# Kernel tuning notes

Measured on AMD Instinct MI355X. Metric: run time of the kernel, lower is better.

Reference implementation:

```python
import jax, jax.numpy as jnp
import numpy as np

DIMS = 256; K = 3; G = 4; CG = DIMS // G; P = K * K
STRIDE = 1; PAD = K // 2; DIL = 1; OFFSET_SCALE = 1.0; SOFTMAX = False
PW_OUT = int(np.ceil(G * P * 3 / 8) * 8)  # 112


def setup_inputs() -> dict:
    key = jax.random.key(0)
    ks = jax.random.split(key, 6)
    N, H, W = 4, 64, 64
    x = jax.random.normal(ks[0], (N, DIMS, H, W), dtype=jnp.float32)
    dw_w = jax.random.normal(ks[1], (DIMS, 1, K, K), dtype=jnp.float32) * 0.1
    dw_b = jnp.zeros((DIMS,), dtype=jnp.float32)
    pw_w = jax.random.normal(ks[2], (PW_OUT, DIMS), dtype=jnp.float32) * 0.01
    pw_b = jnp.zeros((PW_OUT,), dtype=jnp.float32)
    pin_w = jax.random.normal(ks[3], (DIMS, DIMS), dtype=jnp.float32) * (1.0 / np.sqrt(DIMS))
    pin_b = jnp.zeros((DIMS,), dtype=jnp.float32)
    pout_w = jax.random.normal(ks[4], (DIMS, DIMS), dtype=jnp.float32) * (1.0 / np.sqrt(DIMS))
    pout_b = jnp.zeros((DIMS,), dtype=jnp.float32)
    return {"x": x, "dw_w": dw_w, "dw_b": dw_b, "pw_w": pw_w, "pw_b": pw_b,
            "pin_w": pin_w, "pin_b": pin_b, "pout_w": pout_w, "pout_b": pout_b}


def _forward(x, dw_w, dw_b, pw_w, pw_b, pin_w, pin_b, pout_w, pout_b):
    N, C, H, W = x.shape
    L = H * W
    inp = x.reshape(N, C, L).transpose(0, 2, 1)              # [N, L, C]
    # input projection
    val = inp @ pin_w.T + pin_b                               # [N, L, C]
    # offset/mask head: depthwise conv (on raw input) + pointwise linear
    om = jax.lax.conv_general_dilated(
        x, dw_w, window_strides=(1, 1), padding=[(PAD, PAD), (PAD, PAD)],
        dimension_numbers=("NCHW", "OIHW", "NCHW"), feature_group_count=C)
    om = om + dw_b[None, :, None, None]
    om = om.reshape(N, C, L).transpose(0, 2, 1)               # [N, L, C]
    om = om @ pw_w.T + pw_b                                   # [N, L, PW_OUT]
    om = om[..., : G * P * 3].reshape(N, L, G, P, 3)
    off_x = om[..., 0] * OFFSET_SCALE                         # [N, L, G, P]
    off_y = om[..., 1] * OFFSET_SCALE
    mask = om[..., 2]
    if SOFTMAX:
        mask = jax.nn.softmax(mask, axis=-1)
    # kernel grid (P points)
    ky, kx = jnp.meshgrid(jnp.arange(K), jnp.arange(K), indexing="ij")
    ky = (ky.reshape(-1) * DIL).astype(jnp.float32)           # [P]
    kx = (kx.reshape(-1) * DIL).astype(jnp.float32)
    # base output positions (stride 1, zero pad)
    yb = jnp.repeat(jnp.arange(H), W).astype(jnp.float32) * STRIDE - PAD   # [L]
    xb = jnp.tile(jnp.arange(W), H).astype(jnp.float32) * STRIDE - PAD
    pos_y = yb[None, :, None, None] + ky[None, None, None, :] + off_y     # [N,L,G,P]
    pos_x = xb[None, :, None, None] + kx[None, None, None, :] + off_x
    # bilinear gather from grouped value tensor
    vflat = val.reshape(N * L * G, CG)
    n_ids = jnp.arange(N)[:, None, None, None]
    g_ids = jnp.arange(G)[None, None, :, None]

    def gather(iy, ix):
        valid = (iy >= 0) & (iy < H) & (ix >= 0) & (ix < W)
        sidx = jnp.clip(iy, 0, H - 1) * W + jnp.clip(ix, 0, W - 1)
        gidx = (n_ids * L + sidx) * G + g_ids                 # [N,L,G,P]
        v = vflat[gidx]                                       # [N,L,G,P,CG]
        return jnp.where(valid[..., None], v, 0.0)

    y0 = jnp.floor(pos_y); x0 = jnp.floor(pos_x)
    fy = pos_y - y0; fx = pos_x - x0
    iy0 = y0.astype(jnp.int32); ix0 = x0.astype(jnp.int32)
    iy1 = iy0 + 1; ix1 = ix0 + 1
    w00 = (1 - fy) * (1 - fx); w01 = (1 - fy) * fx
    w10 = fy * (1 - fx); w11 = fy * fx
    acc = (jnp.einsum("nlgp,nlgpc->nlgc", mask * w00, gather(iy0, ix0))
           + jnp.einsum("nlgp,nlgpc->nlgc", mask * w01, gather(iy0, ix1))
           + jnp.einsum("nlgp,nlgpc->nlgc", mask * w10, gather(iy1, ix0))
           + jnp.einsum("nlgp,nlgpc->nlgc", mask * w11, gather(iy1, ix1)))
    out = acc.reshape(N, L, C)
    out = out @ pout_w.T + pout_b                             # output projection
    return out.transpose(0, 2, 1).reshape(N, C, H, W)


def reference(x, dw_w, dw_b, pw_w, pw_b, pin_w, pin_b, pout_w, pout_b):
    return _forward(x, dw_w, dw_b, pw_w, pw_b, pin_w, pin_b, pout_w, pout_b)
```

## Files before the change

kernel.cpp:

```cpp
#include <hip/hip_runtime.h>

typedef unsigned short u16;
typedef short bf16x8 __attribute__((ext_vector_type(8)));
typedef u16 u16x8 __attribute__((ext_vector_type(8)));
typedef float f32x4 __attribute__((ext_vector_type(4)));

#define K_DIM 256
#define L_DIM 4096
#define NBATCH 4

static __device__ __forceinline__ u16 f2bf(float f) {
    unsigned u = __float_as_uint(f);
    unsigned r = (u + 0x7FFFu + ((u >> 16) & 1u)) >> 16;
    return (u16)r;
}
static __device__ __forceinline__ float bf2f(u16 v) {
    return __uint_as_float(((unsigned)v) << 16);
}

#define GLOAD16(g, l) __builtin_amdgcn_global_load_lds( \
    (const __attribute__((address_space(1))) void*)(g), \
    (__attribute__((address_space(3))) void*)(l), 16, 0, 0)

__global__ __launch_bounds__(256) void prep_kernel(
    const float* __restrict__ x, const float* __restrict__ dw_w,
    const float* __restrict__ dw_b, const float* __restrict__ pin_w,
    const float* __restrict__ pw_w, const float* __restrict__ pout_w,
    u16* __restrict__ xb_t, u16* __restrict__ dwc_t,
    u16* __restrict__ pin_wb, u16* __restrict__ pw_wb,
    u16* __restrict__ pout_wb)
{
    if (blockIdx.x == 4) {
        if (blockIdx.z != 0) return;
        const int end = (blockIdx.y + 1) * 2560;
        for (int k = blockIdx.y * 2560 + threadIdx.x; k < end; k += 256) {
            if (k < 65536) pin_wb[k] = f2bf(pin_w[k]);
            else if (k < 98304) {
                int j = k - 65536;
                pw_wb[j] = ((j >> 8) < 112) ? f2bf(pw_w[j]) : (u16)0;
            } else {
                int j = k - 98304;
                pout_wb[j] = f2bf(pout_w[j]);
            }
        }
        return;
    }

    __shared__ u16 tx_[64][66];
    __shared__ u16 td_[64][66];
    const int c0 = blockIdx.x * 64, h = blockIdx.y, n = blockIdx.z;
    const int t = threadIdx.x;
    const float* xn = x + (size_t)n * 256 * L_DIM;

    const int w4 = (t & 15) * 4;
    const int cs = t >> 4;

    #pragma unroll
    for (int j = 0; j < 4; ++j) {
        const int cl = cs * 4 + j, c = c0 + cl;
        const float* xc = xn + (size_t)c * L_DIM;
        const float* w9 = dw_w + c * 9;

        float s[4];
        const float bv = dw_b[c];
        #pragma unroll
        for (int k = 0; k < 4; ++k) s[k] = bv;
        f32x4 center;

        #pragma unroll
        for (int dy = 0; dy < 3; ++dy) {
            const int hh = h + dy - 1;
            if (hh < 0 || hh > 63) continue;
            const float* row = xc + hh * 64;
            const f32x4 m = *(const f32x4*)(row + w4);
            const float flv = row[(w4 > 0) ? w4 - 1 : 0];
            const float frv = row[(w4 + 4 < 64) ? w4 + 4 : 63];
            if (dy == 1) center = m;
            #pragma unroll
            for (int k = 0; k < 4; ++k) {
                const int w = w4 + k;
                const float lv = (w > 0) ? 1.f : 0.f;
                const float rv = (w < 63) ? 1.f : 0.f;
                const float xm = (k == 0) ? flv : m[k - 1];
                const float xp = (k == 3) ? frv : m[k + 1];
                s[k] = fmaf(xm * lv, w9[dy*3 + 0], s[k]);
                s[k] = fmaf(m[k],    w9[dy*3 + 1], s[k]);
                s[k] = fmaf(xp * rv, w9[dy*3 + 2], s[k]);
            }
        }
        #pragma unroll
        for (int k = 0; k < 4; ++k) {
            tx_[w4 + k][cl] = f2bf(center[k]);
            td_[w4 + k][cl] = f2bf(s[k]);
        }
    }
    __syncthreads();

    const int cc = t & 63, cq = t >> 6;
    for (int j = 0; j < 16; ++j) {
        const int wl = j * 4 + cq;
        const size_t o = ((size_t)n * L_DIM + h * 64 + wl) * 256 + c0 + cc;
        xb_t[o]  = tx_[wl][cc];
        dwc_t[o] = td_[wl][cc];
    }
}

__global__ __launch_bounds__(256) void gemm_dual(
    const u16* __restrict__ xb_t, const u16* __restrict__ dwc_t,
    const u16* __restrict__ pin_wb, const u16* __restrict__ pw_wb,
    const float* __restrict__ pin_b, const float* __restrict__ pw_b,
    u16* __restrict__ val_b, float* __restrict__ omb)
{
    __shared__ u16 lds[16384];
    const int bx = blockIdx.x;
    const bool isPw = (bx == 2);
    const u16* Ag = isPw ? dwc_t : xb_t;
    const u16* Bg = isPw ? pw_wb : pin_wb;
    const float* bias = isPw ? pw_b : pin_b;
    const int n0 = isPw ? 0 : bx * 128;
    const int Ncols = isPw ? 112 : 256;
    const int ldC = isPw ? 112 : 256;
    const int m0 = blockIdx.y * 128;

    const int t = threadIdx.x;
    const int wave = t >> 6, lane = t & 63;
    const int lr = lane & 15, lk = lane >> 4;
    const int wr = wave >> 1, wc = wave & 1;
    const int wbase = wave << 10;

    const int srow = t >> 2;
    const int scol = (t & 3) * 8;
    const u16* ga0 = Ag + (size_t)(m0 + srow)      * K_DIM + scol;
    const u16* ga1 = Ag + (size_t)(m0 + 64 + srow) * K_DIM + scol;
    const u16* gb0 = Bg + (size_t)(n0 + srow)      * K_DIM + scol;
    const u16* gb1 = Bg + (size_t)(n0 + 64 + srow) * K_DIM + scol;

    f32x4 acc[4][4];
    #pragma unroll
    for (int m = 0; m < 4; ++m)
        #pragma unroll
        for (int n = 0; n < 4; ++n) acc[m][n] = (f32x4){0.f, 0.f, 0.f, 0.f};

    auto stage = [&](int b, int kt) {
        const int ko = kt * 32;
        char* base = (char*)lds + b * 16384 + wbase;
        GLOAD16(ga0 + ko, base);
        GLOAD16(ga1 + ko, base + 4096);
        GLOAD16(gb0 + ko, base + 8192);
        GLOAD16(gb1 + ko, base + 12288);
    };

    stage(0, 0);
    asm volatile("s_waitcnt vmcnt(0)" ::: "memory");
    __syncthreads();

    for (int kt = 0; kt < 8; ++kt) {
        const int cur = kt & 1;
        if (kt < 7) stage(cur ^ 1, kt + 1);
        const char* la = (const char*)lds + cur * 16384;
        const char* lb = la + 8192;
        bf16x8 af[4], bfr[4];
        #pragma unroll
        for (int m = 0; m < 4; ++m)
            af[m] = *(const bf16x8*)(la + ((wr*64 + m*16 + lr) * 32 + lk * 8) * 2);
        #pragma unroll
        for (int n = 0; n < 4; ++n)
            bfr[n] = *(const bf16x8*)(lb + ((wc*64 + n*16 + lr) * 32 + lk * 8) * 2);
        #pragma unroll
        for (int m = 0; m < 4; ++m)
            #pragma unroll
            for (int n = 0; n < 4; ++n)
                acc[m][n] = __builtin_amdgcn_mfma_f32_16x16x32_bf16(
                    af[m], bfr[n], acc[m][n], 0, 0, 0);
        asm volatile("s_waitcnt vmcnt(0)" ::: "memory");
        __syncthreads();
    }

    #pragma unroll
    for (int m = 0; m < 4; ++m) {
        #pragma unroll
        for (int n = 0; n < 4; ++n) {
            const int col = n0 + wc*64 + n*16 + lr;
            if (col < Ncols) {
                const float bv = bias[col];
                #pragma unroll
                for (int r = 0; r < 4; ++r) {
                    const int row = m0 + wr*64 + m*16 + lk*4 + r;
                    const float o = acc[m][n][r] + bv;
                    const size_t off = (size_t)row * ldC + col;
                    if (isPw) omb[off] = o;
                    else      val_b[off] = f2bf(o);
                }
            }
        }
    }
}

__global__ __launch_bounds__(512, 4) void gather_pout(
    const float* __restrict__ om, const u16* __restrict__ val,
    const u16* __restrict__ pout_wb, const float* __restrict__ pout_b,
    float* __restrict__ out)
{
    __shared__ u16 sacc[32][264];
    __shared__ float som[4096];
    const int blk = blockIdx.x;
    const int xcd = blk & 7, s = blk >> 3;
    const int half = s & 1, rd = (s >> 1) & 7, n = s >> 4;
    const int h = xcd * 8 + rd;
    const int l0 = h * 64 + half * 32;
    const int t = threadIdx.x;

    {
        const float* omsrc = om + ((size_t)n * L_DIM + l0) * 112;
        const int wb = (t >> 6) << 10;
        GLOAD16(omsrc + t * 4,        (char*)som + wb);
        GLOAD16(omsrc + 2048 + t * 4, (char*)som + 8192 + wb);
        asm volatile("s_waitcnt vmcnt(0)" ::: "memory");
        __syncthreads();
    }

    {
        const u16* valn = val + (size_t)n * L_DIM * 256;
        const float ybase = (float)h - 1.f;

        #pragma unroll
        for (int i = 0; i < 2; ++i) {
            const int slot = i * 512 + t;
            const int pos = slot >> 5;
            const int g = (slot >> 3) & 3;
            const int ch = (slot & 7) * 8;
            const int l = l0 + pos;
            const float* omp = som + pos * 112 + g * 27;
            const u16* vb = valn + g * 64 + ch;
            const float xb = (float)(l & 63) - 1.f;

            float a[8];
            #pragma unroll
            for (int j = 0; j < 8; ++j) a[j] = 0.f;

            #pragma unroll 3
            for (int p = 0; p < 9; ++p) {
                const float ox = omp[p*3 + 0];
                const float oy = omp[p*3 + 1];
                const float mk = omp[p*3 + 2];
                const float py = ybase + (float)(p / 3) + oy;
                const float px = xb + (float)(p % 3) + ox;
                const float y0 = floorf(py), x0 = floorf(px);
                const float fy = py - y0, fx = px - x0;
                const int iy0 = (int)y0, ix0 = (int)x0;
                const float wy[2] = {mk * (1.f - fy), mk * fy};
                const float wx[2] = {1.f - fx, fx};
                #pragma unroll
                for (int c4 = 0; c4 < 4; ++c4) {
                    const int dy = c4 >> 1, dx = c4 & 1;
                    const int iy = iy0 + dy, ix = ix0 + dx;
                    const bool ok = ((unsigned)iy < 64u) & ((unsigned)ix < 64u);
                    const float wgt = ok ? wy[dy] * wx[dx] : 0.f;
                    const int iyc = min(max(iy, 0), 63);
                    const int ixc = min(max(ix, 0), 63);
                    const u16x8 v = *(const u16x8*)(vb + (size_t)(iyc * 64 + ixc) * 256);
                    #pragma unroll
                    for (int j = 0; j < 8; ++j) a[j] = fmaf(wgt, bf2f(v[j]), a[j]);
                }
            }
            u16x8 o;
            #pragma unroll
            for (int j = 0; j < 8; ++j) o[j] = f2bf(a[j]);
            *(u16x8*)(&sacc[pos][g*64 + ch]) = o;
        }
    }
    __syncthreads();

    const int wave = t >> 6, lane = t & 63;
    const int lr = lane & 15, lk = lane >> 4;

    f32x4 acc4[2][2];
    #pragma unroll
    for (int m = 0; m < 2; ++m)
        #pragma unroll
        for (int nn = 0; nn < 2; ++nn) acc4[m][nn] = (f32x4){0.f, 0.f, 0.f, 0.f};

    #pragma unroll
    for (int kt = 0; kt < 8; ++kt) {
        bf16x8 bfr[2];
        #pragma unroll
        for (int nn = 0; nn < 2; ++nn)
            bfr[nn] = *(const bf16x8*)(&sacc[nn*16 + lr][kt*32 + lk*8]);
        #pragma unroll
        for (int m = 0; m < 2; ++m) {
            const bf16x8 af = *(const bf16x8*)(pout_wb +
                (size_t)(wave*32 + m*16 + lr) * K_DIM + kt*32 + lk*8);
            #pragma unroll
            for (int nn = 0; nn < 2; ++nn)
                acc4[m][nn] = __builtin_amdgcn_mfma_f32_16x16x32_bf16(
                    af, bfr[nn], acc4[m][nn], 0, 0, 0);
        }
    }

    float* outn = out + (size_t)n * 256 * L_DIM;
    #pragma unroll
    for (int m = 0; m < 2; ++m) {
        #pragma unroll
        for (int nn = 0; nn < 2; ++nn) {
            const int col = l0 + nn*16 + lr;
            #pragma unroll
            for (int r = 0; r < 4; ++r) {
                const int row = wave*32 + m*16 + lk*4 + r;
                outn[(size_t)row * L_DIM + col] = acc4[m][nn][r] + pout_b[row];
            }
        }
    }
}

extern "C" void kernel_launch(void* const* d_in, const int* in_sizes, int n_in,
                              void* d_out, int out_size, void* d_ws, size_t ws_size,
                              hipStream_t stream) {
    const float* x      = (const float*)d_in[0];
    const float* dw_w   = (const float*)d_in[1];
    const float* dw_b   = (const float*)d_in[2];
    const float* pw_w   = (const float*)d_in[3];
    const float* pw_b   = (const float*)d_in[4];
    const float* pin_w  = (const float*)d_in[5];
    const float* pin_b  = (const float*)d_in[6];
    const float* pout_w = (const float*)d_in[7];
    const float* pout_b = (const float*)d_in[8];
    float* out = (float*)d_out;

    char* ws = (char*)d_ws;
    u16*   xb_t    = (u16*)ws;
    u16*   dwc_t   = (u16*)(ws + 8388608);
    u16*   val_b   = (u16*)(ws + 16777216);
    float* omb     = (float*)(ws + 25165824);
    u16*   pin_wb  = (u16*)(ws + 32505856);
    u16*   pw_wb   = (u16*)(ws + 32636928);
    u16*   pout_wb = (u16*)(ws + 32702464);

    prep_kernel<<<dim3(5, 64, NBATCH), 256, 0, stream>>>(
        x, dw_w, dw_b, pin_w, pw_w, pout_w,
        xb_t, dwc_t, pin_wb, pw_wb, pout_wb);

    gemm_dual<<<dim3(3, 128), 256, 0, stream>>>(
        xb_t, dwc_t, pin_wb, pw_wb, pin_b, pw_b, val_b, omb);

    gather_pout<<<dim3(512), 512, 0, stream>>>(
        omb, val_b, pout_wb, pout_b, out);
}
```

Before: 58.13 us.

## Fuse offset/mask pointwise GEMM into gather kernel, drop om round-trip

Moves the 112-column pointwise projection of the depthwise conv output out of the dual GEMM kernel and computes it inside gather_pout with MFMA, writing straight to LDS. The input GEMM now launches only the pin-projection blocks. This removes the fp32 om buffer write and reread through global memory and shrinks the GEMM grid, in exchange for extra work and global loads at the start of each gather block, which happen before the gather itself can begin.

```diff
diff --git a/kernel.cpp b/kernel.cpp
--- a/kernel.cpp
+++ b/kernel.cpp
@@ -105,21 +105,12 @@
     }
 }
 
-__global__ __launch_bounds__(256) void gemm_dual(
-    const u16* __restrict__ xb_t, const u16* __restrict__ dwc_t,
-    const u16* __restrict__ pin_wb, const u16* __restrict__ pw_wb,
-    const float* __restrict__ pin_b, const float* __restrict__ pw_b,
-    u16* __restrict__ val_b, float* __restrict__ omb)
+__global__ __launch_bounds__(256) void gemm_pin(
+    const u16* __restrict__ xb_t, const u16* __restrict__ pin_wb,
+    const float* __restrict__ pin_b, u16* __restrict__ val_b)
 {
     __shared__ u16 lds[16384];
-    const int bx = blockIdx.x;
-    const bool isPw = (bx == 2);
-    const u16* Ag = isPw ? dwc_t : xb_t;
-    const u16* Bg = isPw ? pw_wb : pin_wb;
-    const float* bias = isPw ? pw_b : pin_b;
-    const int n0 = isPw ? 0 : bx * 128;
-    const int Ncols = isPw ? 112 : 256;
-    const int ldC = isPw ? 112 : 256;
+    const int n0 = blockIdx.x * 128;
     const int m0 = blockIdx.y * 128;
 
     const int t = threadIdx.x;
@@ -130,10 +121,10 @@
 
     const int srow = t >> 2;
     const int scol = (t & 3) * 8;
-    const u16* ga0 = Ag + (size_t)(m0 + srow)      * K_DIM + scol;
-    const u16* ga1 = Ag + (size_t)(m0 + 64 + srow) * K_DIM + scol;
-    const u16* gb0 = Bg + (size_t)(n0 + srow)      * K_DIM + scol;
-    const u16* gb1 = Bg + (size_t)(n0 + 64 + srow) * K_DIM + scol;
+    const u16* ga0 = xb_t + (size_t)(m0 + srow)      * K_DIM + scol;
+    const u16* ga1 = xb_t + (size_t)(m0 + 64 + srow) * K_DIM + scol;
+    const u16* gb0 = pin_wb + (size_t)(n0 + srow)      * K_DIM + scol;
+    const u16* gb1 = pin_wb + (size_t)(n0 + 64 + srow) * K_DIM + scol;
 
     f32x4 acc[4][4];
     #pragma unroll
@@ -181,43 +172,58 @@
         #pragma unroll
         for (int n = 0; n < 4; ++n) {
             const int col = n0 + wc*64 + n*16 + lr;
-            if (col < Ncols) {
-                const float bv = bias[col];
-                #pragma unroll
-                for (int r = 0; r < 4; ++r) {
-                    const int row = m0 + wr*64 + m*16 + lk*4 + r;
-                    const float o = acc[m][n][r] + bv;
-                    const size_t off = (size_t)row * ldC + col;
-                    if (isPw) omb[off] = o;
-                    else      val_b[off] = f2bf(o);
-                }
+            const float bv = pin_b[col];
+            #pragma unroll
+            for (int r = 0; r < 4; ++r) {
+                const int row = m0 + wr*64 + m*16 + lk*4 + r;
+                val_b[(size_t)row * 256 + col] = f2bf(acc[m][n][r] + bv);
             }
         }
     }
 }
 
 __global__ __launch_bounds__(512, 4) void gather_pout(
-    const float* __restrict__ om, const u16* __restrict__ val,
+    const u16* __restrict__ dwc_t, const u16* __restrict__ val,
+    const u16* __restrict__ pw_wb, const float* __restrict__ pw_b,
     const u16* __restrict__ pout_wb, const float* __restrict__ pout_b,
     float* __restrict__ out)
 {
     __shared__ u16 sacc[32][264];
-    __shared__ float som[4096];
+    __shared__ float som[32 * 112];
     const int blk = blockIdx.x;
     const int xcd = blk & 7, s = blk >> 3;
     const int half = s & 1, rd = (s >> 1) & 7, n = s >> 4;
     const int h = xcd * 8 + rd;
     const int l0 = h * 64 + half * 32;
     const int t = threadIdx.x;
+    const int wave = t >> 6, lane = t & 63;
+    const int lr = lane & 15, lk = lane >> 4;
 
     {
-        const float* omsrc = om + ((size_t)n * L_DIM + l0) * 112;
-        const int wb = (t >> 6) << 10;
-        GLOAD16(omsrc + t * 4,        (char*)som + wb);
-        GLOAD16(omsrc + 2048 + t * 4, (char*)som + 8192 + wb);
-        asm volatile("s_waitcnt vmcnt(0)" ::: "memory");
-        __syncthreads();
-    }
+        const u16* dwcn = dwc_t + ((size_t)n * L_DIM + l0) * 256;
+        #pragma unroll
+        for (int tt = 0; tt < 2; ++tt) {
+            const int T = wave + tt * 8;
+            if (T < 14) {
+                const int m = T & 1, nn = T >> 1;
+                f32x4 acc = (f32x4){0.f, 0.f, 0.f, 0.f};
+                #pragma unroll
+                for (int kt = 0; kt < 8; ++kt) {
+                    const bf16x8 a = *(const bf16x8*)(dwcn +
+                        (size_t)(m*16 + lr) * K_DIM + kt*32 + lk*8);
+                    const bf16x8 b = *(const bf16x8*)(pw_wb +
+                        (size_t)(nn*16 + lr) * K_DIM + kt*32 + lk*8);
+                    acc = __builtin_amdgcn_mfma_f32_16x16x32_bf16(a, b, acc, 0, 0, 0);
+                }
+                const int col = nn*16 + lr;
+                const float bv = pw_b[col];
+                #pragma unroll
+                for (int r = 0; r < 4; ++r)
+                    som[(m*16 + lk*4 + r) * 112 + col] = acc[r] + bv;
+            }
+        }
+    }
+    __syncthreads();
 
     {
         const u16* valn = val + (size_t)n * L_DIM * 256;
@@ -271,9 +277,6 @@
     }
     __syncthreads();
 
-    const int wave = t >> 6, lane = t & 63;
-    const int lr = lane & 15, lk = lane >> 4;
-
     f32x4 acc4[2][2];
     #pragma unroll
     for (int m = 0; m < 2; ++m)
@@ -330,18 +333,17 @@
     u16*   xb_t    = (u16*)ws;
     u16*   dwc_t   = (u16*)(ws + 8388608);
     u16*   val_b   = (u16*)(ws + 16777216);
-    float* omb     = (float*)(ws + 25165824);
-    u16*   pin_wb  = (u16*)(ws + 32505856);
-    u16*   pw_wb   = (u16*)(ws + 32636928);
-    u16*   pout_wb = (u16*)(ws + 32702464);
+    u16*   pin_wb  = (u16*)(ws + 25165824);
+    u16*   pw_wb   = (u16*)(ws + 25296896);
+    u16*   pout_wb = (u16*)(ws + 25362432);
 
     prep_kernel<<<dim3(5, 64, NBATCH), 256, 0, stream>>>(
         x, dw_w, dw_b, pin_w, pw_w, pout_w,
         xb_t, dwc_t, pin_wb, pw_wb, pout_wb);
 
-    gemm_dual<<<dim3(3, 128), 256, 0, stream>>>(
-        xb_t, dwc_t, pin_wb, pw_wb, pin_b, pw_b, val_b, omb);
+    gemm_pin<<<dim3(2, 128), 256, 0, stream>>>(
+        xb_t, pin_wb, pin_b, val_b);
 
     gather_pout<<<dim3(512), 512, 0, stream>>>(
-        omb, val_b, pout_wb, pout_b, out);
-}
+        dwc_t, val_b, pw_wb, pw_b, pout_wb, pout_b, out);
+}
```

New measurement: 65.97 us. +13.5%, slower.

## Split fused gather+output projection into separate gather and tiled GEMM kernels

Applied to the files above, without the earlier changes.

Replaces the fused gather_pout kernel with two kernels. A small-block gather kernel writes bf16 sampled features to a workspace buffer. A separate double-buffered 128x128 MFMA GEMM then applies the output projection. This is meant to raise gather occupancy and to get better weight reuse and LDS staging in the projection GEMM. The cost is an extra global round-trip of an 8 MB intermediate and one more kernel launch.

```diff
diff --git a/kernel.cpp b/kernel.cpp
--- a/kernel.cpp
+++ b/kernel.cpp
@@ -196,117 +196,145 @@
     }
 }
 
-__global__ __launch_bounds__(512, 4) void gather_pout(
+__global__ __launch_bounds__(256, 8) void gather_kernel(
     const float* __restrict__ om, const u16* __restrict__ val,
-    const u16* __restrict__ pout_wb, const float* __restrict__ pout_b,
-    float* __restrict__ out)
+    u16* __restrict__ accb)
 {
-    __shared__ u16 sacc[32][264];
-    __shared__ float som[4096];
+    __shared__ float som[904];
     const int blk = blockIdx.x;
-    const int xcd = blk & 7, s = blk >> 3;
-    const int half = s & 1, rd = (s >> 1) & 7, n = s >> 4;
-    const int h = xcd * 8 + rd;
-    const int l0 = h * 64 + half * 32;
+    const int grp = (blk & 7) * 256 + (blk >> 3);
+    const int n = grp >> 9;
+    const int l0 = (grp & 511) * 8;
     const int t = threadIdx.x;
 
     {
         const float* omsrc = om + ((size_t)n * L_DIM + l0) * 112;
-        const int wb = (t >> 6) << 10;
-        GLOAD16(omsrc + t * 4,        (char*)som + wb);
-        GLOAD16(omsrc + 2048 + t * 4, (char*)som + 8192 + wb);
+        if (t < 224) {
+            const int wb = (t >> 6) << 10;
+            GLOAD16(omsrc + t * 4, (char*)som + wb);
+        }
         asm volatile("s_waitcnt vmcnt(0)" ::: "memory");
         __syncthreads();
     }
 
-    {
-        const u16* valn = val + (size_t)n * L_DIM * 256;
-        const float ybase = (float)h - 1.f;
-
-        #pragma unroll
-        for (int i = 0; i < 2; ++i) {
-            const int slot = i * 512 + t;
-            const int pos = slot >> 5;
-            const int g = (slot >> 3) & 3;
-            const int ch = (slot & 7) * 8;
-            const int l = l0 + pos;
-            const float* omp = som + pos * 112 + g * 27;
-            const u16* vb = valn + g * 64 + ch;
-            const float xb = (float)(l & 63) - 1.f;
-
-            float a[8];
-            #pragma unroll
-            for (int j = 0; j < 8; ++j) a[j] = 0.f;
-
-            #pragma unroll 3
-            for (int p = 0; p < 9; ++p) {
-                const float ox = omp[p*3 + 0];
-                const float oy = omp[p*3 + 1];
-                const float mk = omp[p*3 + 2];
-                const float py = ybase + (float)(p / 3) + oy;
-                const float px = xb + (float)(p % 3) + ox;
-                const float y0 = floorf(py), x0 = floorf(px);
-                const float fy = py - y0, fx = px - x0;
-                const int iy0 = (int)y0, ix0 = (int)x0;
-                const float wy[2] = {mk * (1.f - fy), mk * fy};
-                const float wx[2] = {1.f - fx, fx};
-                #pragma unroll
-                for (int c4 = 0; c4 < 4; ++c4) {
-                    const int dy = c4 >> 1, dx = c4 & 1;
-                    const int iy = iy0 + dy, ix = ix0 + dx;
-                    const bool ok = ((unsigned)iy < 64u) & ((unsigned)ix < 64u);
-                    const float wgt = ok ? wy[dy] * wx[dx] : 0.f;
-                    const int iyc = min(max(iy, 0), 63);
-                    const int ixc = min(max(ix, 0), 63);
-                    const u16x8 v = *(const u16x8*)(vb + (size_t)(iyc * 64 + ixc) * 256);
-                    #pragma unroll
-                    for (int j = 0; j < 8; ++j) a[j] = fmaf(wgt, bf2f(v[j]), a[j]);
-                }
-            }
-            u16x8 o;
-            #pragma unroll
-            for (int j = 0; j < 8; ++j) o[j] = f2bf(a[j]);
-            *(u16x8*)(&sacc[pos][g*64 + ch]) = o;
-        }
-    }
-    __syncthreads();
-
+    const int pos = t >> 5;
+    const int g = (t >> 3) & 3;
+    const int ch = (t & 7) * 8;
+    const int l = l0 + pos;
+    const float* omp = som + pos * 112 + g * 27;
+    const u16* vb = val + (size_t)n * L_DIM * 256 + g * 64 + ch;
+    const float ybase = (float)(l >> 6) - 1.f;
+    const float xb = (float)(l & 63) - 1.f;
+
+    float a[8];
+    #pragma unroll
+    for (int j = 0; j < 8; ++j) a[j] = 0.f;
+
+    #pragma unroll 3
+    for (int p = 0; p < 9; ++p) {
+        const float ox = omp[p*3 + 0];
+        const float oy = omp[p*3 + 1];
+        const float mk = omp[p*3 + 2];
+        const float py = ybase + (float)(p / 3) + oy;
+        const float px = xb + (float)(p % 3) + ox;
+        const float y0 = floorf(py), x0 = floorf(px);
+        const float fy = py - y0, fx = px - x0;
+        const int iy0 = (int)y0, ix0 = (int)x0;
+        const float wy[2] = {mk * (1.f - fy), mk * fy};
+        const float wx[2] = {1.f - fx, fx};
+        #pragma unroll
+        for (int c4 = 0; c4 < 4; ++c4) {
+            const int dy = c4 >> 1, dx = c4 & 1;
+            const int iy = iy0 + dy, ix = ix0 + dx;
+            const bool ok = ((unsigned)iy < 64u) & ((unsigned)ix < 64u);
+            const float wgt = ok ? wy[dy] * wx[dx] : 0.f;
+            const int iyc = min(max(iy, 0), 63);
+            const int ixc = min(max(ix, 0), 63);
+            const u16x8 v = *(const u16x8*)(vb + (size_t)(iyc * 64 + ixc) * 256);
+            #pragma unroll
+            for (int j = 0; j < 8; ++j) a[j] = fmaf(wgt, bf2f(v[j]), a[j]);
+        }
+    }
+    u16x8 o;
+    #pragma unroll
+    for (int j = 0; j < 8; ++j) o[j] = f2bf(a[j]);
+    *(u16x8*)(accb + ((size_t)n * L_DIM + l) * 256 + g * 64 + ch) = o;
+}
+
+__global__ __launch_bounds__(256) void gemm_pout(
+    const u16* __restrict__ accb, const u16* __restrict__ pout_wb,
+    const float* __restrict__ pout_b, float* __restrict__ out)
+{
+    __shared__ u16 lds[16384];
+    const int z = blockIdx.z;
+    const u16* Bg = accb + (size_t)z * L_DIM * 256;
+    const int n0 = blockIdx.x * 128;
+    const int m0 = blockIdx.y * 128;
+
+    const int t = threadIdx.x;
     const int wave = t >> 6, lane = t & 63;
     const int lr = lane & 15, lk = lane >> 4;
-
-    f32x4 acc4[2][2];
-    #pragma unroll
-    for (int m = 0; m < 2; ++m)
-        #pragma unroll
-        for (int nn = 0; nn < 2; ++nn) acc4[m][nn] = (f32x4){0.f, 0.f, 0.f, 0.f};
-
-    #pragma unroll
+    const int wr = wave >> 1, wc = wave & 1;
+    const int wbase = wave << 10;
+
+    const int srow = t >> 2;
+    const int scol = (t & 3) * 8;
+    const u16* ga0 = pout_wb + (size_t)(m0 + srow)      * K_DIM + scol;
+    const u16* ga1 = pout_wb + (size_t)(m0 + 64 + srow) * K_DIM + scol;
+    const u16* gb0 = Bg + (size_t)(n0 + srow)      * K_DIM + scol;
+    const u16* gb1 = Bg + (size_t)(n0 + 64 + srow) * K_DIM + scol;
+
+    f32x4 acc[4][4];
+    #pragma unroll
+    for (int m = 0; m < 4; ++m)
+        #pragma unroll
+        for (int n = 0; n < 4; ++n) acc[m][n] = (f32x4){0.f, 0.f, 0.f, 0.f};
+
+    auto stage = [&](int b, int kt) {
+        const int ko = kt * 32;
+        char* base = (char*)lds + b * 16384 + wbase;
+        GLOAD16(ga0 + ko, base);
+        GLOAD16(ga1 + ko, base + 4096);
+        GLOAD16(gb0 + ko, base + 8192);
+        GLOAD16(gb1 + ko, base + 12288);
+    };
+
+    stage(0, 0);
+    asm volatile("s_waitcnt vmcnt(0)" ::: "memory");
+    __syncthreads();
+
     for (int kt = 0; kt < 8; ++kt) {
-        bf16x8 bfr[2];
-        #pragma unroll
-        for (int nn = 0; nn < 2; ++nn)
-            bfr[nn] = *(const bf16x8*)(&sacc[nn*16 + lr][kt*32 + lk*8]);
-        #pragma unroll
-        for (int m = 0; m < 2; ++m) {
-            const bf16x8 af = *(const bf16x8*)(pout_wb +
-                (size_t)(wave*32 + m*16 + lr) * K_DIM + kt*32 + lk*8);
-            #pragma unroll
-            for (int nn = 0; nn < 2; ++nn)
-                acc4[m][nn] = __builtin_amdgcn_mfma_f32_16x16x32_bf16(
-                    af, bfr[nn], acc4[m][nn], 0, 0, 0);
-        }
-    }
-
-    float* outn = out + (size_t)n * 256 * L_DIM;
-    #pragma unroll
-    for (int m = 0; m < 2; ++m) {
-        #pragma unroll
-        for (int nn = 0; nn < 2; ++nn) {
-            const int col = l0 + nn*16 + lr;
+        const int cur = kt & 1;
+        if (kt < 7) stage(cur ^ 1, kt + 1);
+        const char* la = (const char*)lds + cur * 16384;
+        const char* lb = la + 8192;
+        bf16x8 af[4], bfr[4];
+        #pragma unroll
+        for (int m = 0; m < 4; ++m)
+            af[m] = *(const bf16x8*)(la + ((wr*64 + m*16 + lr) * 32 + lk * 8) * 2);
+        #pragma unroll
+        for (int n = 0; n < 4; ++n)
+            bfr[n] = *(const bf16x8*)(lb + ((wc*64 + n*16 + lr) * 32 + lk * 8) * 2);
+        #pragma unroll
+        for (int m = 0; m < 4; ++m)
+            #pragma unroll
+            for (int n = 0; n < 4; ++n)
+                acc[m][n] = __builtin_amdgcn_mfma_f32_16x16x32_bf16(
+                    af[m], bfr[n], acc[m][n], 0, 0, 0);
+        asm volatile("s_waitcnt vmcnt(0)" ::: "memory");
+        __syncthreads();
+    }
+
+    float* outn = out + (size_t)z * 256 * L_DIM;
+    #pragma unroll
+    for (int m = 0; m < 4; ++m) {
+        #pragma unroll
+        for (int n = 0; n < 4; ++n) {
+            const int col = n0 + wc*64 + n*16 + lr;
             #pragma unroll
             for (int r = 0; r < 4; ++r) {
-                const int row = wave*32 + m*16 + lk*4 + r;
-                outn[(size_t)row * L_DIM + col] = acc4[m][nn][r] + pout_b[row];
+                const int row = m0 + wr*64 + m*16 + lk*4 + r;
+                outn[(size_t)row * L_DIM + col] = acc[m][n][r] + pout_b[row];
             }
         }
     }
@@ -330,10 +358,11 @@
     u16*   xb_t    = (u16*)ws;
     u16*   dwc_t   = (u16*)(ws + 8388608);
     u16*   val_b   = (u16*)(ws + 16777216);
-    float* omb     = (float*)(ws + 25165824);
-    u16*   pin_wb  = (u16*)(ws + 32505856);
-    u16*   pw_wb   = (u16*)(ws + 32636928);
-    u16*   pout_wb = (u16*)(ws + 32702464);
+    u16*   acc_b   = (u16*)(ws + 25165824);
+    float* omb     = (float*)(ws + 33554432);
+    u16*   pin_wb  = (u16*)(ws + 40894464);
+    u16*   pw_wb   = (u16*)(ws + 41025536);
+    u16*   pout_wb = (u16*)(ws + 41091072);
 
     prep_kernel<<<dim3(5, 64, NBATCH), 256, 0, stream>>>(
         x, dw_w, dw_b, pin_w, pw_w, pout_w,
@@ -342,6 +371,8 @@
     gemm_dual<<<dim3(3, 128), 256, 0, stream>>>(
         xb_t, dwc_t, pin_wb, pw_wb, pin_b, pw_b, val_b, omb);
 
-    gather_pout<<<dim3(512), 512, 0, stream>>>(
-        omb, val_b, pout_wb, pout_b, out);
-}
+    gather_kernel<<<dim3(2048), 256, 0, stream>>>(omb, val_b, acc_b);
+
+    gemm_pout<<<dim3(32, 2, NBATCH), 256, 0, stream>>>(
+        acc_b, pout_wb, pout_b, out);
+}
```

Result: no change. 58.63 us (+0.9%).
